# Kernel optimization log

Measured on AMD Instinct MI355X. Metric: run time of the kernel, lower is better.

Reference implementation:

```python
import jax, jax.numpy as jnp
import numpy as np

M = 24      # number of DeepGravity sub-models
D_IN = 495  # input feature dim
H = 64      # hidden dim
L = 5       # hidden layers per sub-model


def setup_inputs() -> dict:
    key = jax.random.key(0)
    ks = jax.random.split(key, 7)
    s = 1.0 / np.sqrt(D_IN)
    sh = 1.0 / np.sqrt(H)
    return {
        "x": jax.random.normal(ks[0], (65536, D_IN), dtype=jnp.float32),
        "W_in": jax.random.uniform(ks[1], (M, D_IN, H), jnp.float32, -s, s),
        "b_in": jax.random.uniform(ks[2], (M, H), jnp.float32, -s, s),
        "W_h": jax.random.uniform(ks[3], (M, L, H, H), jnp.float32, -sh, sh),
        "b_h": jax.random.uniform(ks[4], (M, L, H), jnp.float32, -sh, sh),
        "W_out": jax.random.uniform(ks[5], (M, H), jnp.float32, -sh, sh),
        "b_out": jax.random.uniform(ks[6], (M,), jnp.float32, -sh, sh),
    }


def reference(x, W_in, b_in, W_h, b_h, W_out, b_out):
    # Batched input projection across all 24 models: [M, N, H]
    h0 = jnp.einsum("nf,mfh->mnh", x, W_in) + b_in[:, None, :]
    h = h0
    # 5 hidden layers (fixed, structurally distinct weights) as batched GEMMs
    for l in range(L):
        h = jax.nn.relu(jnp.einsum("mnh,mhk->mnk", h, W_h[:, l]) + b_h[:, l][:, None, :])
    h = h + h0  # residual
    # output head: Linear(64,1) + tanh, squeezed -> [M, N]
    out = jnp.tanh(jnp.einsum("mnh,mh->mn", h, W_out) + b_out[:, None])
    return out.T  # [N, M]
```

## Files before the change

kernel.cpp:

```cpp
#include <hip/hip_runtime.h>
#include <hip/hip_bf16.h>

typedef __attribute__((ext_vector_type(8))) short short8;
typedef __attribute__((ext_vector_type(4))) float f32x4;
typedef __attribute__((ext_vector_type(4))) unsigned uint4v;

#define NMODEL 24
#define DIN    495
#define KP     512
#define HID    64
#define NLAY   5

__device__ __forceinline__ short bf16r(float f) {
    unsigned u = __float_as_uint(f);
    u += 0x7fffu + ((u >> 16) & 1u);
    return (short)(u >> 16);
}
__device__ __forceinline__ float bf16f(short s) {
    return __uint_as_float(((unsigned)(unsigned short)s) << 16);
}
__device__ __forceinline__ unsigned pkbf16(float lo, float hi) {
    unsigned r;
    asm("v_cvt_pk_bf16_f32 %0, %1, %2" : "=v"(r) : "v"(lo), "v"(hi));
    return r;
}
__device__ __forceinline__ short8 pack2(f32x4 a, f32x4 b) {
    uint4v w;
    w[0] = pkbf16(a[0], a[1]);
    w[1] = pkbf16(a[2], a[3]);
    w[2] = pkbf16(b[0], b[1]);
    w[3] = pkbf16(b[2], b[3]);
    return __builtin_bit_cast(short8, w);
}

struct __attribute__((packed, aligned(4))) f4a { float v[4]; };

__global__ void dg_convert(const float* __restrict__ W_in,
                           const float* __restrict__ W_h,
                           short* __restrict__ wib, short* __restrict__ whb) {
    int idx = blockIdx.x * 256 + threadIdx.x;
    if (idx < NMODEL * 64 * HID * 8) {
        int t    = idx & 7;
        int hout = (idx >> 3) & 63;
        int kb   = (idx >> 9) & 63;
        int m    = idx >> 15;
        int k    = kb * 8 + t;
        float v  = (k < DIN) ? W_in[((size_t)m * DIN + k) * HID + hout] : 0.f;
        wib[idx] = bf16r(v);
    }
    if (idx < NMODEL * NLAY * 8 * HID * 8) {
        int t    = idx & 7;
        int hout = (idx >> 3) & 63;
        int kb   = (idx >> 9) & 7;
        int ml   = idx >> 12;
        int pk   = 16 * (2 * (kb >> 2) + (t >> 2)) + 4 * (kb & 3) + (t & 3);
        float v  = W_h[((size_t)ml * HID + pk) * HID + hout];
        whb[idx] = bf16r(v);
    }
}

__global__ __launch_bounds__(512, 4) void dg_main(
    const float* __restrict__ x,
    const short* __restrict__ wib, const short* __restrict__ whb,
    const float* __restrict__ b_in, const float* __restrict__ b_h,
    const float* __restrict__ W_out, const float* __restrict__ b_out,
    float* __restrict__ out) {

    __shared__ short xs[64 * KP];

    const int tid  = threadIdx.x;
    const int lane = tid & 63;
    const int w    = tid >> 6;
    const int lrow = lane & 15;
    const int g    = lane >> 4;
    const int rowbase = blockIdx.x * 64;

    for (int i = 0; i < 8; ++i) {
        int r  = i * 8 + w;
        int k0 = lane * 8;
        const float* xr = x + (size_t)(rowbase + r) * DIN + k0;
        uint4v vw;
        if (k0 + 8 <= DIN) {
            f4a a = *(const f4a*)xr;
            f4a b = *(const f4a*)(xr + 4);
            vw[0] = pkbf16(a.v[0], a.v[1]);
            vw[1] = pkbf16(a.v[2], a.v[3]);
            vw[2] = pkbf16(b.v[0], b.v[1]);
            vw[3] = pkbf16(b.v[2], b.v[3]);
        } else {
            float f[8];
#pragma unroll
            for (int j = 0; j < 8; ++j) f[j] = (k0 + j < DIN) ? xr[j] : 0.f;
            vw[0] = pkbf16(f[0], f[1]);
            vw[1] = pkbf16(f[2], f[3]);
            vw[2] = pkbf16(f[4], f[5]);
            vw[3] = pkbf16(f[6], f[7]);
        }
        int byte = (r * (KP * 2) + k0 * 2) ^ ((r & 7) << 4);
        *(short8*)((char*)xs + byte) = __builtin_bit_cast(short8, vw);
    }
    __syncthreads();

    for (int mi = 0; mi < 3; ++mi) {
        const int m = mi * 8 + w;

        f32x4 acc[4][4];
#pragma unroll
        for (int a = 0; a < 4; ++a)
#pragma unroll
            for (int b = 0; b < 4; ++b) acc[a][b] = (f32x4)0.0f;

        const short8* wA = (const short8*)wib + (size_t)m * 64 * 64;
#pragma unroll 2
        for (int skt = 0; skt < 16; ++skt) {
            const int kb = skt * 4 + g;
            short8 afr[4], bfr[4];
#pragma unroll
            for (int icf = 0; icf < 4; ++icf)
                afr[icf] = wA[(size_t)kb * 64 + icf * 16 + lrow];
#pragma unroll
            for (int rf = 0; rf < 4; ++rf) {
                int r = rf * 16 + lrow;
                int byte = (r * (KP * 2) + skt * 64 + g * 16) ^ ((r & 7) << 4);
                bfr[rf] = *(const short8*)((const char*)xs + byte);
            }
#pragma unroll
            for (int icf = 0; icf < 4; ++icf)
#pragma unroll
                for (int rf = 0; rf < 4; ++rf)
                    acc[icf][rf] = __builtin_amdgcn_mfma_f32_16x16x32_bf16(
                        afr[icf], bfr[rf], acc[icf][rf], 0, 0, 0);
        }

        const float* bi = b_in + m * HID;
#pragma unroll
        for (int icf = 0; icf < 4; ++icf) {
            f32x4 bv = *(const f32x4*)(bi + icf * 16 + g * 4);
#pragma unroll
            for (int rf = 0; rf < 4; ++rf) acc[icf][rf] += bv;
        }

        short8 h0b[2][4];
#pragma unroll
        for (int s = 0; s < 2; ++s)
#pragma unroll
            for (int rf = 0; rf < 4; ++rf)
                h0b[s][rf] = pack2(acc[2 * s][rf], acc[2 * s + 1][rf]);

        const short8* wH = (const short8*)whb + (size_t)m * NLAY * 8 * 64;
        short8 hc[2][4];
#pragma unroll
        for (int s = 0; s < 2; ++s)
#pragma unroll
            for (int rf = 0; rf < 4; ++rf) hc[s][rf] = h0b[s][rf];

        f32x4 hacc[4][4];
        for (int l = 0; l < NLAY; ++l) {
#pragma unroll
            for (int a = 0; a < 4; ++a)
#pragma unroll
                for (int b = 0; b < 4; ++b) hacc[a][b] = (f32x4)0.0f;
#pragma unroll
            for (int s = 0; s < 2; ++s) {
                const int kb = 4 * s + g;
                short8 afr[4];
#pragma unroll
                for (int icf = 0; icf < 4; ++icf)
                    afr[icf] = wH[(size_t)(l * 8 + kb) * 64 + icf * 16 + lrow];
#pragma unroll
                for (int icf = 0; icf < 4; ++icf)
#pragma unroll
                    for (int rf = 0; rf < 4; ++rf)
                        hacc[icf][rf] = __builtin_amdgcn_mfma_f32_16x16x32_bf16(
                            afr[icf], hc[s][rf], hacc[icf][rf], 0, 0, 0);
            }
            const float* bh = b_h + (size_t)(m * NLAY + l) * HID;
#pragma unroll
            for (int icf = 0; icf < 4; ++icf) {
                f32x4 bv = *(const f32x4*)(bh + icf * 16 + g * 4);
#pragma unroll
                for (int rf = 0; rf < 4; ++rf)
#pragma unroll
                    for (int j = 0; j < 4; ++j)
                        hacc[icf][rf][j] = fmaxf(hacc[icf][rf][j] + bv[j], 0.f);
            }
            if (l != NLAY - 1) {
#pragma unroll
                for (int s = 0; s < 2; ++s)
#pragma unroll
                    for (int rf = 0; rf < 4; ++rf)
                        hc[s][rf] = pack2(hacc[2 * s][rf], hacc[2 * s + 1][rf]);
            }
        }

#pragma unroll
        for (int icf = 0; icf < 4; ++icf)
#pragma unroll
            for (int rf = 0; rf < 4; ++rf)
#pragma unroll
                for (int j = 0; j < 4; ++j)
                    hacc[icf][rf][j] += bf16f(h0b[icf >> 1][rf][(icf & 1) * 4 + j]);

        const float* wo = W_out + m * HID;
        f32x4 wov[4];
#pragma unroll
        for (int icf = 0; icf < 4; ++icf)
            wov[icf] = *(const f32x4*)(wo + icf * 16 + g * 4);
        const float bo = b_out[m];
#pragma unroll
        for (int rf = 0; rf < 4; ++rf) {
            float s = 0.f;
#pragma unroll
            for (int icf = 0; icf < 4; ++icf)
#pragma unroll
                for (int j = 0; j < 4; ++j)
                    s += hacc[icf][rf][j] * wov[icf][j];
            s += __shfl_xor(s, 16);
            s += __shfl_xor(s, 32);
            s += bo;
            float e = __expf(2.f * s);
            float o = 1.f - 2.f / (e + 1.f);
            if (g == 0)
                out[(size_t)(rowbase + rf * 16 + lrow) * NMODEL + m] = o;
        }
    }
}

extern "C" void kernel_launch(void* const* d_in, const int* in_sizes, int n_in,
                              void* d_out, int out_size, void* d_ws, size_t ws_size,
                              hipStream_t stream) {
    const float* x     = (const float*)d_in[0];
    const float* W_in  = (const float*)d_in[1];
    const float* b_in  = (const float*)d_in[2];
    const float* W_h   = (const float*)d_in[3];
    const float* b_h   = (const float*)d_in[4];
    const float* W_out = (const float*)d_in[5];
    const float* b_out = (const float*)d_in[6];
    float* out = (float*)d_out;

    short* wib = (short*)d_ws;
    short* whb = wib + NMODEL * 64 * HID * 8;

    const int N = in_sizes[0] / DIN;

    dg_convert<<<3072, 256, 0, stream>>>(W_in, W_h, wib, whb);
    dg_main<<<N / 64, 512, 0, stream>>>(x, wib, whb, b_in, b_h, W_out, b_out, out);
}
```

Baseline: 242.6 us.

## Split each model's hidden dim across wave pairs with LDS-exchanged activations

Blocks grow from 512 to 1024 threads. Each pair of waves shares one model, and each wave computes half of the 64 hidden outputs. Hidden activations are written to LDS as bf16 and read back as the MFMA B operand, with block-wide barriers between layers. Output-head partial sums are combined through LDS, biases are folded into the accumulator init, and MFMA sections get raised wave priority. This halves per-wave accumulator registers to raise parallelism, at the cost of 136KB of dynamic LDS per block, which allows one block per CU, plus many full-block __syncthreads.

```diff
diff --git a/kernel.cpp b/kernel.cpp
--- a/kernel.cpp
+++ b/kernel.cpp
@@ -31,6 +31,14 @@
     w[2] = pkbf16(b[0], b[1]);
     w[3] = pkbf16(b[2], b[3]);
     return __builtin_bit_cast(short8, w);
+}
+__device__ __forceinline__ void wr_h(char* hb, int row, int col, f32x4 v) {
+    unsigned d0 = pkbf16(v[0], v[1]);
+    unsigned d1 = pkbf16(v[2], v[3]);
+    int byte = (row * 128 + col * 2) ^ ((row & 7) << 4);
+    unsigned long long q = (unsigned long long)d0 |
+                           ((unsigned long long)d1 << 32);
+    *(unsigned long long*)(hb + byte) = q;
 }
 
 struct __attribute__((packed, aligned(4))) f4a { float v[4]; };
@@ -53,20 +61,20 @@
         int hout = (idx >> 3) & 63;
         int kb   = (idx >> 9) & 7;
         int ml   = idx >> 12;
-        int pk   = 16 * (2 * (kb >> 2) + (t >> 2)) + 4 * (kb & 3) + (t & 3);
-        float v  = W_h[((size_t)ml * HID + pk) * HID + hout];
-        whb[idx] = bf16r(v);
-    }
-}
-
-__global__ __launch_bounds__(512, 4) void dg_main(
+        int k    = kb * 8 + t;
+        whb[idx] = bf16r(W_h[((size_t)ml * HID + k) * HID + hout]);
+    }
+}
+
+__global__ __launch_bounds__(1024, 4) void dg_main(
     const float* __restrict__ x,
     const short* __restrict__ wib, const short* __restrict__ whb,
     const float* __restrict__ b_in, const float* __restrict__ b_h,
     const float* __restrict__ W_out, const float* __restrict__ b_out,
     float* __restrict__ out) {
 
-    __shared__ short xs[64 * KP];
+    extern __shared__ char lds[];
+    short* xs = (short*)lds;
 
     const int tid  = threadIdx.x;
     const int lane = tid & 63;
@@ -74,9 +82,13 @@
     const int lrow = lane & 15;
     const int g    = lane >> 4;
     const int rowbase = blockIdx.x * 64;
-
-    for (int i = 0; i < 8; ++i) {
-        int r  = i * 8 + w;
+    const int pairI = w >> 1;
+    const int hh    = w & 1;
+    char*  hb = lds + 65536 + pairI * 8192;
+    float* pb = (float*)(lds + 131072 + pairI * 512);
+
+    for (int i = 0; i < 4; ++i) {
+        int r  = i * 16 + w;
         int k0 = lane * 8;
         const float* xr = x + (size_t)(rowbase + r) * DIN + k0;
         uint4v vw;
@@ -101,128 +113,148 @@
     }
     __syncthreads();
 
+#pragma unroll 1
     for (int mi = 0; mi < 3; ++mi) {
-        const int m = mi * 8 + w;
-
-        f32x4 acc[4][4];
-#pragma unroll
-        for (int a = 0; a < 4; ++a)
-#pragma unroll
-            for (int b = 0; b < 4; ++b) acc[a][b] = (f32x4)0.0f;
-
-        const short8* wA = (const short8*)wib + (size_t)m * 64 * 64;
+        const int m = pairI * 3 + mi;
+
+        const float* bi = b_in + m * HID + hh * 32;
+        f32x4 acc[2][4];
+#pragma unroll
+        for (int icf = 0; icf < 2; ++icf) {
+            f32x4 bv = *(const f32x4*)(bi + icf * 16 + g * 4);
+#pragma unroll
+            for (int rf = 0; rf < 4; ++rf) acc[icf][rf] = bv;
+        }
+
+        const short8* wA = (const short8*)wib + (size_t)m * 4096;
 #pragma unroll 2
         for (int skt = 0; skt < 16; ++skt) {
             const int kb = skt * 4 + g;
-            short8 afr[4], bfr[4];
-#pragma unroll
-            for (int icf = 0; icf < 4; ++icf)
-                afr[icf] = wA[(size_t)kb * 64 + icf * 16 + lrow];
+            short8 afr[2], bfr[4];
+#pragma unroll
+            for (int icf = 0; icf < 2; ++icf)
+                afr[icf] = wA[(size_t)kb * 64 + hh * 32 + icf * 16 + lrow];
 #pragma unroll
             for (int rf = 0; rf < 4; ++rf) {
                 int r = rf * 16 + lrow;
                 int byte = (r * (KP * 2) + skt * 64 + g * 16) ^ ((r & 7) << 4);
                 bfr[rf] = *(const short8*)((const char*)xs + byte);
             }
-#pragma unroll
-            for (int icf = 0; icf < 4; ++icf)
+            __builtin_amdgcn_s_setprio(1);
+#pragma unroll
+            for (int icf = 0; icf < 2; ++icf)
 #pragma unroll
                 for (int rf = 0; rf < 4; ++rf)
                     acc[icf][rf] = __builtin_amdgcn_mfma_f32_16x16x32_bf16(
                         afr[icf], bfr[rf], acc[icf][rf], 0, 0, 0);
-        }
-
-        const float* bi = b_in + m * HID;
-#pragma unroll
-        for (int icf = 0; icf < 4; ++icf) {
-            f32x4 bv = *(const f32x4*)(bi + icf * 16 + g * 4);
-#pragma unroll
-            for (int rf = 0; rf < 4; ++rf) acc[icf][rf] += bv;
-        }
-
-        short8 h0b[2][4];
-#pragma unroll
-        for (int s = 0; s < 2; ++s)
+            __builtin_amdgcn_s_setprio(0);
+        }
+
+        short8 h0b[4];
+#pragma unroll
+        for (int rf = 0; rf < 4; ++rf)
+            h0b[rf] = pack2(acc[0][rf], acc[1][rf]);
+#pragma unroll
+        for (int icf = 0; icf < 2; ++icf)
 #pragma unroll
             for (int rf = 0; rf < 4; ++rf)
-                h0b[s][rf] = pack2(acc[2 * s][rf], acc[2 * s + 1][rf]);
-
-        const short8* wH = (const short8*)whb + (size_t)m * NLAY * 8 * 64;
-        short8 hc[2][4];
-#pragma unroll
-        for (int s = 0; s < 2; ++s)
-#pragma unroll
-            for (int rf = 0; rf < 4; ++rf) hc[s][rf] = h0b[s][rf];
-
-        f32x4 hacc[4][4];
+                wr_h(hb, rf * 16 + lrow, hh * 32 + icf * 16 + g * 4,
+                     acc[icf][rf]);
+        __syncthreads();
+
+        const short8* wHm = (const short8*)whb + (size_t)m * 2560;
+        f32x4 ha[2][4];
+#pragma unroll 1
         for (int l = 0; l < NLAY; ++l) {
-#pragma unroll
-            for (int a = 0; a < 4; ++a)
-#pragma unroll
-                for (int b = 0; b < 4; ++b) hacc[a][b] = (f32x4)0.0f;
+            const float* bh = b_h + (size_t)(m * NLAY + l) * HID + hh * 32;
+#pragma unroll
+            for (int icf = 0; icf < 2; ++icf) {
+                f32x4 bv = *(const f32x4*)(bh + icf * 16 + g * 4);
+#pragma unroll
+                for (int rf = 0; rf < 4; ++rf) ha[icf][rf] = bv;
+            }
 #pragma unroll
             for (int s = 0; s < 2; ++s) {
                 const int kb = 4 * s + g;
-                short8 afr[4];
-#pragma unroll
-                for (int icf = 0; icf < 4; ++icf)
-                    afr[icf] = wH[(size_t)(l * 8 + kb) * 64 + icf * 16 + lrow];
-#pragma unroll
-                for (int icf = 0; icf < 4; ++icf)
+                short8 afr[2], bfr[4];
+#pragma unroll
+                for (int icf = 0; icf < 2; ++icf)
+                    afr[icf] = wHm[(size_t)(l * 8 + kb) * 64 +
+                                   hh * 32 + icf * 16 + lrow];
+#pragma unroll
+                for (int rf = 0; rf < 4; ++rf) {
+                    int r = rf * 16 + lrow;
+                    int byte = (r * 128 + kb * 16) ^ ((r & 7) << 4);
+                    bfr[rf] = *(const short8*)(hb + byte);
+                }
+                __builtin_amdgcn_s_setprio(1);
+#pragma unroll
+                for (int icf = 0; icf < 2; ++icf)
 #pragma unroll
                     for (int rf = 0; rf < 4; ++rf)
-                        hacc[icf][rf] = __builtin_amdgcn_mfma_f32_16x16x32_bf16(
-                            afr[icf], hc[s][rf], hacc[icf][rf], 0, 0, 0);
-            }
-            const float* bh = b_h + (size_t)(m * NLAY + l) * HID;
-#pragma unroll
-            for (int icf = 0; icf < 4; ++icf) {
-                f32x4 bv = *(const f32x4*)(bh + icf * 16 + g * 4);
+                        ha[icf][rf] = __builtin_amdgcn_mfma_f32_16x16x32_bf16(
+                            afr[icf], bfr[rf], ha[icf][rf], 0, 0, 0);
+                __builtin_amdgcn_s_setprio(0);
+            }
+#pragma unroll
+            for (int icf = 0; icf < 2; ++icf)
 #pragma unroll
                 for (int rf = 0; rf < 4; ++rf)
 #pragma unroll
                     for (int j = 0; j < 4; ++j)
-                        hacc[icf][rf][j] = fmaxf(hacc[icf][rf][j] + bv[j], 0.f);
-            }
+                        ha[icf][rf][j] = fmaxf(ha[icf][rf][j], 0.f);
             if (l != NLAY - 1) {
-#pragma unroll
-                for (int s = 0; s < 2; ++s)
+                __syncthreads();
+#pragma unroll
+                for (int icf = 0; icf < 2; ++icf)
 #pragma unroll
                     for (int rf = 0; rf < 4; ++rf)
-                        hc[s][rf] = pack2(hacc[2 * s][rf], hacc[2 * s + 1][rf]);
-            }
-        }
-
-#pragma unroll
-        for (int icf = 0; icf < 4; ++icf)
+                        wr_h(hb, rf * 16 + lrow, hh * 32 + icf * 16 + g * 4,
+                             ha[icf][rf]);
+                __syncthreads();
+            }
+        }
+
+#pragma unroll
+        for (int icf = 0; icf < 2; ++icf)
 #pragma unroll
             for (int rf = 0; rf < 4; ++rf)
 #pragma unroll
                 for (int j = 0; j < 4; ++j)
-                    hacc[icf][rf][j] += bf16f(h0b[icf >> 1][rf][(icf & 1) * 4 + j]);
-
-        const float* wo = W_out + m * HID;
-        f32x4 wov[4];
-#pragma unroll
-        for (int icf = 0; icf < 4; ++icf)
-            wov[icf] = *(const f32x4*)(wo + icf * 16 + g * 4);
-        const float bo = b_out[m];
+                    ha[icf][rf][j] += bf16f(h0b[rf][icf * 4 + j]);
+
+        const float* wo = W_out + m * HID + hh * 32;
+        float hp[4];
 #pragma unroll
         for (int rf = 0; rf < 4; ++rf) {
             float s = 0.f;
 #pragma unroll
-            for (int icf = 0; icf < 4; ++icf)
+            for (int icf = 0; icf < 2; ++icf) {
+                f32x4 wv = *(const f32x4*)(wo + icf * 16 + g * 4);
 #pragma unroll
                 for (int j = 0; j < 4; ++j)
-                    s += hacc[icf][rf][j] * wov[icf][j];
+                    s += ha[icf][rf][j] * wv[j];
+            }
             s += __shfl_xor(s, 16);
             s += __shfl_xor(s, 32);
-            s += bo;
-            float e = __expf(2.f * s);
-            float o = 1.f - 2.f / (e + 1.f);
-            if (g == 0)
-                out[(size_t)(rowbase + rf * 16 + lrow) * NMODEL + m] = o;
-        }
+            hp[rf] = s;
+        }
+        if (g == 0) {
+#pragma unroll
+            for (int rf = 0; rf < 4; ++rf)
+                pb[hh * 64 + rf * 16 + lrow] = hp[rf];
+        }
+        __syncthreads();
+        {
+            int r = hh * 32 + (lane & 31);
+            if (lane < 32) {
+                float s = pb[r] + pb[64 + r] + b_out[m];
+                float e = __expf(2.f * s);
+                float o = 1.f - 2.f / (e + 1.f);
+                out[(size_t)(rowbase + r) * NMODEL + m] = o;
+            }
+        }
+        __syncthreads();
     }
 }
 
@@ -242,7 +274,12 @@
     short* whb = wib + NMODEL * 64 * HID * 8;
 
     const int N = in_sizes[0] / DIN;
+    const int LDS_BYTES = 65536 + 65536 + 4096;
+
+    hipFuncSetAttribute((const void*)dg_main,
+                        hipFuncAttributeMaxDynamicSharedMemorySize, LDS_BYTES);
 
     dg_convert<<<3072, 256, 0, stream>>>(W_in, W_h, wib, whb);
-    dg_main<<<N / 64, 512, 0, stream>>>(x, wib, whb, b_in, b_h, W_out, b_out, out);
-}
+    dg_main<<<N / 64, 1024, LDS_BYTES, stream>>>(x, wib, whb, b_in, b_h,
+                                                 W_out, b_out, out);
+}
```

After: 225.9 us. 1.07x faster.
